# Kernel optimization log

Hardware: AMD Instinct MI355X
Metric: run time of the kernel (lower is better)

The kernel has to match this reference:

```python
import jax, jax.numpy as jnp
import numpy as np

BATCH, SEQ = 256, 100
DM = 256           # d_m
DI = 512           # Mamba d_inner = 2*d_m
DID = 512          # decoder d_inner = 2*d_d
N = 16             # d_state
DTR = 16           # dt_rank = ceil(d_m/16)
DCONV = 4
NLAYERS = 3


def silu(v):
    return v * jax.nn.sigmoid(v)


def setup_inputs() -> dict:
    key = jax.random.key(0)
    ks = jax.random.split(key, 20)
    rn = lambda k, s, sc=0.02: jax.random.normal(k, s, jnp.float32) * sc
    A_log = jnp.log(jnp.arange(1, N + 1, dtype=jnp.float32))  # (N,)
    return {
        'x': jax.random.normal(ks[0], (BATCH, SEQ, 8), jnp.float32),
        'W_embed': rn(ks[1], (8, DM)), 'b_embed': jnp.zeros((DM,), jnp.float32),
        'm_in_w': rn(ks[2], (DM, 2 * DI)),
        'm_conv_w': rn(ks[3], (DI, DCONV), 0.1), 'm_conv_b': jnp.zeros((DI,), jnp.float32),
        'm_xproj_w': rn(ks[4], (DI, DTR + 2 * N)),
        'm_dtproj_w': rn(ks[5], (DTR, DI), DTR ** -0.5),
        'm_dtproj_b': rn(ks[6], (DI,), 0.5) - 4.0,
        'm_A_log': jnp.broadcast_to(A_log, (DI, N)).copy(),
        'm_D': jnp.ones((DI,), jnp.float32),
        'm_out_w': rn(ks[7], (DI, DM)),
        'dec_in_w': rn(ks[8], (NLAYERS, 4, 2 * DID)), 'dec_in_b': jnp.zeros((NLAYERS, 2 * DID), jnp.float32),
        'dec_flow_w': rn(ks[9], (NLAYERS, DM, DTR + 2 * N)),
        'dec_dt_w': rn(ks[10], (NLAYERS, DTR, DID), DTR ** -0.5),
        'dec_dt_b': rn(ks[11], (NLAYERS, DID), 0.5) - 4.0,
        'dec_A_log': jnp.broadcast_to(A_log, (NLAYERS, DID, N)).copy(),
        'dec_D': jnp.ones((NLAYERS, DID), jnp.float32),
        'dec_out_w': rn(ks[12], (NLAYERS, DID, 4)), 'dec_out_b': jnp.zeros((NLAYERS, 4), jnp.float32),
    }


def _forward(x, W_embed, b_embed, m_in_w, m_conv_w, m_conv_b, m_xproj_w,
             m_dtproj_w, m_dtproj_b, m_A_log, m_D, m_out_w,
             dec_in_w, dec_in_b, dec_flow_w, dec_dt_w, dec_dt_b,
             dec_A_log, dec_D, dec_out_w, dec_out_b):
    b, l, _ = x.shape
    # ---- MambaEncoder ----
    emb = x @ W_embed + b_embed                       # (b, l, dm)
    xz = emb @ m_in_w                                 # (b, l, 2*di)
    xs, z = jnp.split(xz, 2, axis=-1)
    # causal depthwise conv1d, kernel=DCONV
    xp = jnp.pad(xs, ((0, 0), (DCONV - 1, 0), (0, 0)))
    xc = sum(xp[:, k:k + l, :] * m_conv_w[:, k] for k in range(DCONV)) + m_conv_b
    xc = silu(xc)
    proj = xc @ m_xproj_w                             # (b, l, dtr+2n)
    dt = jax.nn.softplus(proj[..., :DTR] @ m_dtproj_w + m_dtproj_b)  # (b, l, di)
    Bm = proj[..., DTR:DTR + N]                       # (b, l, n)
    Cm = proj[..., DTR + N:]
    A = -jnp.exp(m_A_log)                             # (di, n)

    def enc_step(h, inp):
        dt_t, B_t, C_t, x_t = inp                     # (b,di),(b,n),(b,n),(b,di)
        h = h * jnp.exp(dt_t[:, :, None] * A) + (dt_t * x_t)[:, :, None] * B_t[:, None, :]
        y = jnp.einsum('bdn,bn->bd', h, C_t) + m_D * x_t
        return h, y

    h0 = jnp.zeros((b, DI, N), xc.dtype)
    _, ys = jax.lax.scan(enc_step, h0,
                         (dt.transpose(1, 0, 2), Bm.transpose(1, 0, 2),
                          Cm.transpose(1, 0, 2), xc.transpose(1, 0, 2)))
    y = ys.transpose(1, 0, 2) * silu(z)               # (b, l, di)
    enc = y @ m_out_w                                 # (b, l, dm)
    flow = enc[:, -1]                                 # (b, dm) -- last token (no cls_token)

    # ---- FlowDecoder stack ----
    cur_bbox = x[:, -1, :4]
    hidden = jnp.zeros((b, DID, N), x.dtype)

    def dec_step(carry, p):
        bbox, h = carry
        in_w, in_b, flow_w, dt_w, dt_b, A_log, Dp, out_w, out_b = p
        bh = bbox @ in_w + in_b                       # (b, 2*did)
        e, r = jnp.split(bh, 2, axis=-1)
        e = silu(e)
        pf = flow @ flow_w                            # (b, dtr+2n)
        dtd = jax.nn.softplus(pf[:, :DTR] @ dt_w + dt_b)  # (b, did)
        Bp, Cp = pf[:, DTR:DTR + N], pf[:, DTR + N:]
        Ad = -jnp.exp(A_log)                          # (did, n)
        h = h * jnp.exp(dtd[:, :, None] * Ad) + e[:, :, None] * (dtd[:, :, None] * Bp[:, None, :])
        yd = jnp.einsum('bdn,bn->bd', h, Cp) + Dp * e
        yd = yd * silu(r)
        out = yd @ out_w + out_b                      # (b, 4)
        # torch code detaches cur_bbox and hidden_state between layers
        return (jax.lax.stop_gradient(out), jax.lax.stop_gradient(h)), out

    _, outs = jax.lax.scan(dec_step, (cur_bbox, hidden),
                           (dec_in_w, dec_in_b, dec_flow_w, dec_dt_w, dec_dt_b,
                            dec_A_log, dec_D, dec_out_w, dec_out_b))
    return outs[-1]                                   # final predicted bbox (b, 4)


def reference(x, W_embed, b_embed, m_in_w, m_conv_w, m_conv_b, m_xproj_w,
              m_dtproj_w, m_dtproj_b, m_A_log, m_D, m_out_w,
              dec_in_w, dec_in_b, dec_flow_w, dec_dt_w, dec_dt_b,
              dec_A_log, dec_D, dec_out_w, dec_out_b):
    return _forward(x, W_embed, b_embed, m_in_w, m_conv_w, m_conv_b, m_xproj_w,
                    m_dtproj_w, m_dtproj_b, m_A_log, m_D, m_out_w,
                    dec_in_w, dec_in_b, dec_flow_w, dec_dt_w, dec_dt_b,
                    dec_A_log, dec_D, dec_out_w, dec_out_b)
```

## Files before the change

kernel.cpp:

```cpp
#include <hip/hip_runtime.h>
#include <math.h>

#define BATCH 256
#define SEQ 100
#define DMODEL 256
#define DI 512
#define DID 512
#define NST 16
#define DTRANK 16
#define DCONV 4
#define NLAYERS 3

#define W2_OFF 0
#define B2_OFF 8192
#define WT_OFF 9216
#define CWT_OFF 33792
#define FLAG_OFF 35840
#define PROJ_OFF 35848
#define SILUZ_OFF 1264648
#define Y_OFF 1395720

__device__ __forceinline__ float silu_f(float x) { return x / (1.0f + __expf(-x)); }
__device__ __forceinline__ float softplus_f(float x) {
    return fmaxf(x, 0.0f) + __logf(1.0f + __expf(-fabsf(x)));
}

#define DPP_ADD(v, ctrl, rmask) \
    v += __int_as_float(__builtin_amdgcn_update_dpp(0, __float_as_int(v), ctrl, rmask, 0xF, false))

__device__ __forceinline__ float wave64_sum(float v) {
    DPP_ADD(v, 0xB1, 0xF);
    DPP_ADD(v, 0x4E, 0xF);
    DPP_ADD(v, 0x141, 0xF);
    DPP_ADD(v, 0x140, 0xF);
    DPP_ADD(v, 0x142, 0xA);
    DPP_ADD(v, 0x143, 0xC);
    return v;
}

__global__ void k_prep(const float* __restrict__ W_embed, const float* __restrict__ b_embed,
                       const float* __restrict__ m_in_w, const float* __restrict__ xproj_w,
                       const float* __restrict__ conv_w, const float* __restrict__ A_log,
                       const float* __restrict__ dec_A_log, float* __restrict__ ws,
                       int* __restrict__ flags) {
    int bid = blockIdx.x, tid = threadIdx.x;
    if (bid < 4) {
        int j = bid * 256 + tid;
        float acc[8] = {0, 0, 0, 0, 0, 0, 0, 0};
        float accb = 0.f;
        for (int c = 0; c < DMODEL; ++c) {
            float w = m_in_w[c * 1024 + j];
            accb += b_embed[c] * w;
#pragma unroll
            for (int i = 0; i < 8; ++i) acc[i] += W_embed[i * DMODEL + c] * w;
        }
#pragma unroll
        for (int i = 0; i < 8; ++i) ws[W2_OFF + i * 1024 + j] = acc[i];
        ws[B2_OFF + j] = accb;
    } else if (bid < 100) {
        int idx = (bid - 4) * 256 + tid;
        int j = idx / 512, c = idx % 512;
        ws[WT_OFF + j * 512 + c] = xproj_w[c * 48 + j];
    } else if (bid < 108) {
        int idx = (bid - 100) * 256 + tid;
        int tap = idx / 512, c = idx % 512;
        ws[CWT_OFF + tap * 512 + c] = conv_w[c * 4 + tap];
    } else {
        __shared__ int oks[2];
        if (tid == 0) { oks[0] = 1; oks[1] = 1; }
        __syncthreads();
        int bad_e = 0, bad_d = 0;
        for (int i = tid; i < DI * NST; i += 256) {
            int dd = i / NST, n = i % NST;
            float a0 = __expf(A_log[dd * NST]);
            float an = __expf(A_log[dd * NST + n]);
            if (fabsf(an - (n + 1) * a0) > 1e-4f * (n + 1)) bad_e = 1;
        }
        for (int i = tid; i < NLAYERS * DID * NST; i += 256) {
            int dd = i / NST, n = i % NST;
            float a0 = __expf(dec_A_log[dd * NST]);
            float an = __expf(dec_A_log[dd * NST + n]);
            if (fabsf(an - (n + 1) * a0) > 1e-4f * (n + 1)) bad_d = 1;
        }
        if (bad_e) atomicAnd(&oks[0], 0);
        if (bad_d) atomicAnd(&oks[1], 0);
        __syncthreads();
        if (tid == 0) { flags[0] = oks[0]; flags[1] = oks[1]; }
    }
}

__global__ void __launch_bounds__(256, 3) k_convproj(
    const float* __restrict__ x, const float* __restrict__ ws, const float* __restrict__ conv_b,
    float* __restrict__ proj_g, float* __restrict__ silu_z) {
    __shared__ __align__(16) float xs_s[23 * 512];
    __shared__ __align__(16) float proj_s[20 * 48];
    const float* W2 = ws + W2_OFF;
    const float* b2 = ws + B2_OFF;
    const float* wT = ws + WT_OFF;
    const float* cwT = ws + CWT_OFF;
    const int b = blockIdx.x / 5, tb = blockIdx.x % 5, t0 = tb * 20;
    const int tid = threadIdx.x, lane = tid & 63, wv = tid >> 6;

    {
        int c0 = tid, c1 = tid + 256;
        float wa[8], wb[8];
#pragma unroll
        for (int i = 0; i < 8; ++i) {
            wa[i] = W2[i * 1024 + c0];
            wb[i] = W2[i * 1024 + c1];
        }
        float ba = b2[c0], bbv = b2[c1];
        for (int r = 0; r < 23; ++r) {
            int t = t0 - 3 + r;
            float va = 0.f, vb = 0.f;
            if (t >= 0) {
                const float4* xr = (const float4*)(x + (size_t)(b * SEQ + t) * 8);
                float4 xlo = xr[0], xhi = xr[1];
                va = ba + xlo.x * wa[0] + xlo.y * wa[1] + xlo.z * wa[2] + xlo.w * wa[3] +
                     xhi.x * wa[4] + xhi.y * wa[5] + xhi.z * wa[6] + xhi.w * wa[7];
                vb = bbv + xlo.x * wb[0] + xlo.y * wb[1] + xlo.z * wb[2] + xlo.w * wb[3] +
                     xhi.x * wb[4] + xhi.y * wb[5] + xhi.z * wb[6] + xhi.w * wb[7];
            }
            xs_s[r * 512 + c0] = va;
            xs_s[r * 512 + c1] = vb;
        }
        if (tb == 4) {
            const float4* xr = (const float4*)(x + (size_t)(b * SEQ + SEQ - 1) * 8);
            float4 xlo = xr[0], xhi = xr[1];
            float za = b2[512 + c0], zb = b2[512 + c1];
#pragma unroll
            for (int i = 0; i < 8; ++i) {
                float xi = (i < 4) ? ((const float*)&xlo)[i] : ((const float*)&xhi)[i - 4];
                za += xi * W2[i * 1024 + 512 + c0];
                zb += xi * W2[i * 1024 + 512 + c1];
            }
            silu_z[b * DI + c0] = silu_f(za);
            silu_z[b * DI + c1] = silu_f(zb);
        }
    }
    __syncthreads();
    {
        float cwr[8][4], cbr[8];
#pragma unroll
        for (int k = 0; k < 8; ++k) {
            int c = lane + 64 * k;
#pragma unroll
            for (int tap = 0; tap < 4; ++tap) cwr[k][tap] = cwT[tap * 512 + c];
            cbr[k] = conv_b[c];
        }
        float xcv[5][8];
#pragma unroll
        for (int q = 0; q < 5; ++q) {
            int rb = wv * 5 + q;
#pragma unroll
            for (int k = 0; k < 8; ++k) {
                int c = lane + 64 * k;
                float a = cbr[k];
#pragma unroll
                for (int tap = 0; tap < 4; ++tap) a += cwr[k][tap] * xs_s[(rb + tap) * 512 + c];
                xcv[q][k] = silu_f(a);
            }
        }
        for (int j = 0; j < 48; ++j) {
            float wj[8];
#pragma unroll
            for (int k = 0; k < 8; ++k) wj[k] = wT[j * 512 + lane + 64 * k];
            float a0 = 0, a1 = 0, a2 = 0, a3 = 0, a4 = 0;
#pragma unroll
            for (int k = 0; k < 8; ++k) {
                float w = wj[k];
                a0 += xcv[0][k] * w;
                a1 += xcv[1][k] * w;
                a2 += xcv[2][k] * w;
                a3 += xcv[3][k] * w;
                a4 += xcv[4][k] * w;
            }
            a0 = wave64_sum(a0); a1 = wave64_sum(a1); a2 = wave64_sum(a2);
            a3 = wave64_sum(a3); a4 = wave64_sum(a4);
            if (lane == 63) {
                proj_s[(wv * 5 + 0) * 48 + j] = a0;
                proj_s[(wv * 5 + 1) * 48 + j] = a1;
                proj_s[(wv * 5 + 2) * 48 + j] = a2;
                proj_s[(wv * 5 + 3) * 48 + j] = a3;
                proj_s[(wv * 5 + 4) * 48 + j] = a4;
            }
        }
    }
    __syncthreads();
    if (tid < 240) {
        float4* dst = (float4*)(proj_g + (size_t)(b * SEQ + t0) * 48);
        dst[tid] = ((const float4*)proj_s)[tid];
    }
}

__global__ void __launch_bounds__(512, 4) k_scan(
    const float* __restrict__ x, const float* __restrict__ ws, const float* __restrict__ conv_b,
    const float* __restrict__ proj_g, const float* __restrict__ A_log,
    const float* __restrict__ dtw, const float* __restrict__ dtb,
    const float* __restrict__ Dvec, const float* __restrict__ silu_z,
    const int* __restrict__ flags, float* __restrict__ y_g) {
    __shared__ __align__(16) float proj_l[SEQ * 48];
    __shared__ __align__(16) float x_l[SEQ * 8];
    __shared__ __align__(16) float h1_s[256 * 16];
    const int b = blockIdx.x >> 1, dgrp = blockIdx.x & 1;
    const int tid = threadIdx.x, half = tid >> 8, dl = tid & 255;
    const int d = dgrp * 256 + dl;
    const float* W2 = ws + W2_OFF;
    const float* b2 = ws + B2_OFF;
    const float* cwT = ws + CWT_OFF;

    for (int i = tid; i < SEQ * 48; i += 512) proj_l[i] = proj_g[(size_t)b * SEQ * 48 + i];
    for (int i = tid; i < SEQ * 8; i += 512) x_l[i] = x[(size_t)b * SEQ * 8 + i];

    float w2c[8];
#pragma unroll
    for (int i = 0; i < 8; ++i) w2c[i] = W2[i * 1024 + d];
    float biasc = b2[d];
    float cw0 = cwT[d], cw1 = cwT[512 + d], cw2 = cwT[1024 + d], cw3 = cwT[1536 + d];
    float cb = conv_b[d];
    float wr[DTRANK];
#pragma unroll
    for (int r = 0; r < DTRANK; ++r) wr[r] = dtw[r * DI + d];
    float bdt = dtb[d];
    float An0 = -__expf(A_log[d * NST]);
    const bool fast = flags[0] != 0;
    float h[NST];
#pragma unroll
    for (int n = 0; n < NST; ++n) h[n] = 0.f;
    float S = 0.f, xcv = 0.f;
    const int tstart = half * 50, tend = tstart + 50;
    __syncthreads();

    float win0 = 0.f, win1 = 0.f, win2 = 0.f;
    for (int tt = tstart - 3; tt < tstart; ++tt) {
        float v = 0.f;
        if (tt >= 0) {
            const float4* xr = (const float4*)&x_l[tt * 8];
            float4 xa = xr[0], xb4 = xr[1];
            v = biasc + xa.x * w2c[0] + xa.y * w2c[1] + xa.z * w2c[2] + xa.w * w2c[3] +
                xb4.x * w2c[4] + xb4.y * w2c[5] + xb4.z * w2c[6] + xb4.w * w2c[7];
        }
        win0 = win1; win1 = win2; win2 = v;
    }

    for (int t = tstart; t < tend; ++t) {
        const float4* xr = (const float4*)&x_l[t * 8];
        float4 xa = xr[0], xb4 = xr[1];
        float xsv = biasc + xa.x * w2c[0] + xa.y * w2c[1] + xa.z * w2c[2] + xa.w * w2c[3] +
                    xb4.x * w2c[4] + xb4.y * w2c[5] + xb4.z * w2c[6] + xb4.w * w2c[7];
        float cv = cb + win0 * cw0 + win1 * cw1 + win2 * cw2 + xsv * cw3;
        win0 = win1; win1 = win2; win2 = xsv;
        xcv = silu_f(cv);
        const float* pr = &proj_l[t * 48];
        float4 p0 = *(const float4*)&pr[0];
        float4 p1 = *(const float4*)&pr[4];
        float4 p2 = *(const float4*)&pr[8];
        float4 p3 = *(const float4*)&pr[12];
        float acc = bdt;
        acc += p0.x * wr[0] + p0.y * wr[1] + p0.z * wr[2] + p0.w * wr[3];
        acc += p1.x * wr[4] + p1.y * wr[5] + p1.z * wr[6] + p1.w * wr[7];
        acc += p2.x * wr[8] + p2.y * wr[9] + p2.z * wr[10] + p2.w * wr[11];
        acc += p3.x * wr[12] + p3.y * wr[13] + p3.z * wr[14] + p3.w * wr[15];
        float dtv = softplus_f(acc);
        S += dtv;
        float s = dtv * xcv;
        float4 B0 = *(const float4*)&pr[16];
        float4 B1 = *(const float4*)&pr[20];
        float4 B2 = *(const float4*)&pr[24];
        float4 B3 = *(const float4*)&pr[28];
        float Bv[NST] = {B0.x, B0.y, B0.z, B0.w, B1.x, B1.y, B1.z, B1.w,
                         B2.x, B2.y, B2.z, B2.w, B3.x, B3.y, B3.z, B3.w};
        if (fast) {
            float E = __expf(dtv * An0);
            float Ek = 1.f;
#pragma unroll
            for (int n = 0; n < NST; ++n) {
                Ek *= E;
                h[n] = h[n] * Ek + s * Bv[n];
            }
        } else {
#pragma unroll
            for (int n = 0; n < NST; ++n) {
                float Ann = -__expf(A_log[d * NST + n]);
                h[n] = h[n] * __expf(dtv * Ann) + s * Bv[n];
            }
        }
    }
    if (half == 0) {
#pragma unroll
        for (int n = 0; n < NST; n += 4)
            *(float4*)&h1_s[dl * 16 + n] = make_float4(h[n], h[n + 1], h[n + 2], h[n + 3]);
    }
    __syncthreads();
    if (half == 1) {
        const float* pr = &proj_l[(SEQ - 1) * 48];
        float yv = Dvec[d] * xcv;
        if (fast) {
            float Gb = __expf(S * An0), Gk = 1.f;
#pragma unroll
            for (int n = 0; n < NST; ++n) {
                Gk *= Gb;
                float hf = h[n] + Gk * h1_s[dl * 16 + n];
                yv += hf * pr[32 + n];
            }
        } else {
#pragma unroll
            for (int n = 0; n < NST; ++n) {
                float Ann = -__expf(A_log[d * NST + n]);
                float hf = h[n] + __expf(S * Ann) * h1_s[dl * 16 + n];
                yv += hf * pr[32 + n];
            }
        }
        y_g[(size_t)b * DI + d] = yv * silu_z[(size_t)b * DI + d];
    }
}

__global__ void __launch_bounds__(512, 2) k_flowdec(
    const float* __restrict__ x, const float* __restrict__ y_g,
    const float* __restrict__ m_out_w, const float* __restrict__ dec_in_w,
    const float* __restrict__ dec_in_b, const float* __restrict__ dec_flow_w,
    const float* __restrict__ dec_dt_w, const float* __restrict__ dec_dt_b,
    const float* __restrict__ dec_A_log, const float* __restrict__ dec_D,
    const float* __restrict__ dec_out_w, const float* __restrict__ dec_out_b,
    const int* __restrict__ flags, float* __restrict__ out) {
    __shared__ __align__(16) float y_s[DI];
    __shared__ __align__(16) float pf_s[48];
    __shared__ float red_s[DMODEL];
    __shared__ float flow_s[DMODEL];
    __shared__ float bbox_s[4];
    __shared__ float dred_s[8][4];
    const int b = blockIdx.x, tid = threadIdx.x, d = tid;
    const int lane = tid & 63, wv = tid >> 6;
    const bool dfast = flags[1] != 0;
    y_s[d] = y_g[(size_t)b * DI + d];
    if (tid < 4) bbox_s[tid] = x[(size_t)(b * SEQ + SEQ - 1) * 8 + tid];
    __syncthreads();
    {
        int j = tid >> 1, p = tid & 1;
        float fa = 0.f;
#pragma unroll 4
        for (int i = 0; i < 64; ++i) {
            int c = p * 256 + 4 * i;
            float4 yq = *(const float4*)&y_s[c];
            fa += yq.x * m_out_w[(c + 0) * DMODEL + j];
            fa += yq.y * m_out_w[(c + 1) * DMODEL + j];
            fa += yq.z * m_out_w[(c + 2) * DMODEL + j];
            fa += yq.w * m_out_w[(c + 3) * DMODEL + j];
        }
        if (p == 1) red_s[j] = fa;
        __syncthreads();
        if (p == 0) flow_s[j] = fa + red_s[j];
    }
    float h[NST];
#pragma unroll
    for (int n = 0; n < NST; ++n) h[n] = 0.f;
    __syncthreads();
    for (int L = 0; L < NLAYERS; ++L) {
        float epre = dec_in_b[L * 1024 + d];
        float rpre = dec_in_b[L * 1024 + 512 + d];
#pragma unroll
        for (int i = 0; i < 4; ++i) {
            float bx = bbox_s[i];
            epre += bx * dec_in_w[(L * 4 + i) * 1024 + d];
            rpre += bx * dec_in_w[(L * 4 + i) * 1024 + 512 + d];
        }
        float e = silu_f(epre);
        float fl4[4];
#pragma unroll
        for (int k = 0; k < 4; ++k) fl4[k] = flow_s[lane + 64 * k];
        float pj[6];
#pragma unroll
        for (int jj = 0; jj < 6; ++jj) {
            float a = 0.f;
#pragma unroll
            for (int k = 0; k < 4; ++k)
                a += fl4[k] * dec_flow_w[L * DMODEL * 48 + (lane + 64 * k) * 48 + wv * 6 + jj];
            pj[jj] = wave64_sum(a);
        }
        if (lane == 63) {
#pragma unroll
            for (int jj = 0; jj < 6; ++jj) pf_s[wv * 6 + jj] = pj[jj];
        }
        __syncthreads();
        float4 p0 = *(const float4*)&pf_s[0];
        float4 p1 = *(const float4*)&pf_s[4];
        float4 p2 = *(const float4*)&pf_s[8];
        float4 p3 = *(const float4*)&pf_s[12];
        float dtd = dec_dt_b[L * DID + d];
        dtd += p0.x * dec_dt_w[(L * 16 + 0) * DID + d] + p0.y * dec_dt_w[(L * 16 + 1) * DID + d] +
               p0.z * dec_dt_w[(L * 16 + 2) * DID + d] + p0.w * dec_dt_w[(L * 16 + 3) * DID + d];
        dtd += p1.x * dec_dt_w[(L * 16 + 4) * DID + d] + p1.y * dec_dt_w[(L * 16 + 5) * DID + d] +
               p1.z * dec_dt_w[(L * 16 + 6) * DID + d] + p1.w * dec_dt_w[(L * 16 + 7) * DID + d];
        dtd += p2.x * dec_dt_w[(L * 16 + 8) * DID + d] + p2.y * dec_dt_w[(L * 16 + 9) * DID + d] +
               p2.z * dec_dt_w[(L * 16 + 10) * DID + d] + p2.w * dec_dt_w[(L * 16 + 11) * DID + d];
        dtd += p3.x * dec_dt_w[(L * 16 + 12) * DID + d] + p3.y * dec_dt_w[(L * 16 + 13) * DID + d] +
               p3.z * dec_dt_w[(L * 16 + 14) * DID + d] + p3.w * dec_dt_w[(L * 16 + 15) * DID + d];
        dtd = softplus_f(dtd);
        float4 B0 = *(const float4*)&pf_s[16];
        float4 B1 = *(const float4*)&pf_s[20];
        float4 B2 = *(const float4*)&pf_s[24];
        float4 B3 = *(const float4*)&pf_s[28];
        float4 C0 = *(const float4*)&pf_s[32];
        float4 C1 = *(const float4*)&pf_s[36];
        float4 C2 = *(const float4*)&pf_s[40];
        float4 C3 = *(const float4*)&pf_s[44];
        float Bv[NST] = {B0.x, B0.y, B0.z, B0.w, B1.x, B1.y, B1.z, B1.w,
                         B2.x, B2.y, B2.z, B2.w, B3.x, B3.y, B3.z, B3.w};
        float Cv[NST] = {C0.x, C0.y, C0.z, C0.w, C1.x, C1.y, C1.z, C1.w,
                         C2.x, C2.y, C2.z, C2.w, C3.x, C3.y, C3.z, C3.w};
        float yd = 0.f;
        if (dfast) {
            float Ad0 = -__expf(dec_A_log[(L * DID + d) * NST]);
            float E = __expf(dtd * Ad0), Ek = 1.f;
#pragma unroll
            for (int n = 0; n < NST; ++n) {
                Ek *= E;
                h[n] = h[n] * Ek + e * (dtd * Bv[n]);
                yd += h[n] * Cv[n];
            }
        } else {
#pragma unroll
            for (int n = 0; n < NST; ++n) {
                float Adn = -__expf(dec_A_log[(L * DID + d) * NST + n]);
                h[n] = h[n] * __expf(dtd * Adn) + e * (dtd * Bv[n]);
                yd += h[n] * Cv[n];
            }
        }
        yd += dec_D[L * DID + d] * e;
        yd *= silu_f(rpre);
#pragma unroll
        for (int jo = 0; jo < 4; ++jo) {
            float v = wave64_sum(yd * dec_out_w[(L * DID + d) * 4 + jo]);
            if (lane == 63) dred_s[wv][jo] = v;
        }
        __syncthreads();
        if (tid < 4) {
            float a2 = dec_out_b[L * 4 + tid];
#pragma unroll
            for (int w = 0; w < 8; ++w) a2 += dred_s[w][tid];
            bbox_s[tid] = a2;
            if (L == NLAYERS - 1) out[b * 4 + tid] = a2;
        }
        __syncthreads();
    }
}

extern "C" void kernel_launch(void* const* d_in, const int* in_sizes, int n_in,
                              void* d_out, int out_size, void* d_ws, size_t ws_size,
                              hipStream_t stream) {
    const float* x          = (const float*)d_in[0];
    const float* W_embed    = (const float*)d_in[1];
    const float* b_embed    = (const float*)d_in[2];
    const float* m_in_w     = (const float*)d_in[3];
    const float* m_conv_w   = (const float*)d_in[4];
    const float* m_conv_b   = (const float*)d_in[5];
    const float* m_xproj_w  = (const float*)d_in[6];
    const float* m_dtproj_w = (const float*)d_in[7];
    const float* m_dtproj_b = (const float*)d_in[8];
    const float* m_A_log    = (const float*)d_in[9];
    const float* m_D        = (const float*)d_in[10];
    const float* m_out_w    = (const float*)d_in[11];
    const float* dec_in_w   = (const float*)d_in[12];
    const float* dec_in_b   = (const float*)d_in[13];
    const float* dec_flow_w = (const float*)d_in[14];
    const float* dec_dt_w   = (const float*)d_in[15];
    const float* dec_dt_b   = (const float*)d_in[16];
    const float* dec_A_log  = (const float*)d_in[17];
    const float* dec_D      = (const float*)d_in[18];
    const float* dec_out_w  = (const float*)d_in[19];
    const float* dec_out_b  = (const float*)d_in[20];

    float* ws = (float*)d_ws;
    int* flags = (int*)(ws + FLAG_OFF);
    float* proj_g = ws + PROJ_OFF;
    float* siluz = ws + SILUZ_OFF;
    float* y_g = ws + Y_OFF;

    k_prep<<<109, 256, 0, stream>>>(W_embed, b_embed, m_in_w, m_xproj_w, m_conv_w,
                                    m_A_log, dec_A_log, ws, flags);
    k_convproj<<<BATCH * 5, 256, 0, stream>>>(x, ws, m_conv_b, proj_g, siluz);
    k_scan<<<BATCH * 2, 512, 0, stream>>>(x, ws, m_conv_b, proj_g, m_A_log, m_dtproj_w,
                                          m_dtproj_b, m_D, siluz, flags, y_g);
    k_flowdec<<<BATCH, 512, 0, stream>>>(x, y_g, m_out_w, dec_in_w, dec_in_b, dec_flow_w,
                                         dec_dt_w, dec_dt_b, dec_A_log, dec_D, dec_out_w,
                                         dec_out_b, flags, (float*)d_out);
}
```

Baseline: 155.0 us.

## Stream scan operands via scalar loads, vectorize convproj, tree power chains

The scan kernel no longer stages proj and x in shared memory. It streams each timestep's projection row and input row into SGPRs with double-buffered inline-asm s_load instructions, removing the block-wide staging and the barrier before the scan. The conv/projection kernel switches to float2/float4 vectorized loads and LDS accesses with a new channel-to-lane mapping. The serial Ek*=E power chains are replaced by a tree of products to shorten dependency chains, softplus is simplified to a thresholded form, and the h1_s buffer is padded to 17 floats per row to avoid bank conflicts. Hand-written asm with manual lgkmcnt waits adds fragility and SGPR pressure, and the softplus threshold slightly changes numerics.

```diff
diff --git a/kernel.cpp b/kernel.cpp
--- a/kernel.cpp
+++ b/kernel.cpp
@@ -21,9 +21,6 @@
 #define Y_OFF 1395720
 
 __device__ __forceinline__ float silu_f(float x) { return x / (1.0f + __expf(-x)); }
-__device__ __forceinline__ float softplus_f(float x) {
-    return fmaxf(x, 0.0f) + __logf(1.0f + __expf(-fabsf(x)));
-}
 
 #define DPP_ADD(v, ctrl, rmask) \
     v += __int_as_float(__builtin_amdgcn_update_dpp(0, __float_as_int(v), ctrl, rmask, 0xF, false))
@@ -37,6 +34,26 @@
     DPP_ADD(v, 0x143, 0xC);
     return v;
 }
+
+typedef float sf16 __attribute__((ext_vector_type(16)));
+typedef float sf8 __attribute__((ext_vector_type(8)));
+
+__device__ __forceinline__ int rfl(int v) { return __builtin_amdgcn_readfirstlane(v); }
+
+#define SL2(dA, dB, base, offA, offB)                    \
+    asm volatile("s_load_dwordx16 %0, %2, %3\n\t"        \
+                 "s_load_dwordx16 %1, %2, %4"            \
+                 : "=&s"(dA), "=&s"(dB)                  \
+                 : "s"(base), "s"(offA), "s"(offB))
+#define SLX(dX, base, off) \
+    asm volatile("s_load_dwordx8 %0, %1, %2" : "=&s"(dX) : "s"(base), "s"(off))
+#define SLC(dC, base, off) \
+    asm volatile("s_load_dwordx16 %0, %1, %2" : "=&s"(dC) : "s"(base), "s"(off))
+#define SL_WAIT()                                          \
+    do {                                                   \
+        asm volatile("s_waitcnt lgkmcnt(0)" ::: "memory"); \
+        __builtin_amdgcn_sched_barrier(0);                 \
+    } while (0)
 
 __global__ void k_prep(const float* __restrict__ W_embed, const float* __restrict__ b_embed,
                        const float* __restrict__ m_in_w, const float* __restrict__ xproj_w,
@@ -102,78 +119,89 @@
     const int tid = threadIdx.x, lane = tid & 63, wv = tid >> 6;
 
     {
-        int c0 = tid, c1 = tid + 256;
+        int c0 = tid * 2;
         float wa[8], wb[8];
 #pragma unroll
         for (int i = 0; i < 8; ++i) {
-            wa[i] = W2[i * 1024 + c0];
-            wb[i] = W2[i * 1024 + c1];
-        }
-        float ba = b2[c0], bbv = b2[c1];
+            float2 wp = *(const float2*)&W2[i * 1024 + c0];
+            wa[i] = wp.x;
+            wb[i] = wp.y;
+        }
+        float2 bp = *(const float2*)&b2[c0];
         for (int r = 0; r < 23; ++r) {
             int t = t0 - 3 + r;
             float va = 0.f, vb = 0.f;
             if (t >= 0) {
                 const float4* xr = (const float4*)(x + (size_t)(b * SEQ + t) * 8);
                 float4 xlo = xr[0], xhi = xr[1];
-                va = ba + xlo.x * wa[0] + xlo.y * wa[1] + xlo.z * wa[2] + xlo.w * wa[3] +
+                va = bp.x + xlo.x * wa[0] + xlo.y * wa[1] + xlo.z * wa[2] + xlo.w * wa[3] +
                      xhi.x * wa[4] + xhi.y * wa[5] + xhi.z * wa[6] + xhi.w * wa[7];
-                vb = bbv + xlo.x * wb[0] + xlo.y * wb[1] + xlo.z * wb[2] + xlo.w * wb[3] +
+                vb = bp.y + xlo.x * wb[0] + xlo.y * wb[1] + xlo.z * wb[2] + xlo.w * wb[3] +
                      xhi.x * wb[4] + xhi.y * wb[5] + xhi.z * wb[6] + xhi.w * wb[7];
             }
-            xs_s[r * 512 + c0] = va;
-            xs_s[r * 512 + c1] = vb;
+            *(float2*)&xs_s[r * 512 + c0] = make_float2(va, vb);
         }
         if (tb == 4) {
             const float4* xr = (const float4*)(x + (size_t)(b * SEQ + SEQ - 1) * 8);
             float4 xlo = xr[0], xhi = xr[1];
-            float za = b2[512 + c0], zb = b2[512 + c1];
+            float za = b2[512 + c0], zb = b2[512 + c0 + 1];
 #pragma unroll
             for (int i = 0; i < 8; ++i) {
                 float xi = (i < 4) ? ((const float*)&xlo)[i] : ((const float*)&xhi)[i - 4];
-                za += xi * W2[i * 1024 + 512 + c0];
-                zb += xi * W2[i * 1024 + 512 + c1];
+                float2 wp = *(const float2*)&W2[i * 1024 + 512 + c0];
+                za += xi * wp.x;
+                zb += xi * wp.y;
             }
             silu_z[b * DI + c0] = silu_f(za);
-            silu_z[b * DI + c1] = silu_f(zb);
+            silu_z[b * DI + c0 + 1] = silu_f(zb);
         }
     }
     __syncthreads();
+    const int cA = lane * 4, cB = 256 + lane * 4;
+    float xcv[5][8];
     {
-        float cwr[8][4], cbr[8];
-#pragma unroll
-        for (int k = 0; k < 8; ++k) {
-            int c = lane + 64 * k;
-#pragma unroll
-            for (int tap = 0; tap < 4; ++tap) cwr[k][tap] = cwT[tap * 512 + c];
-            cbr[k] = conv_b[c];
-        }
-        float xcv[5][8];
+        float4 cwA[4], cwB[4];
+#pragma unroll
+        for (int tap = 0; tap < 4; ++tap) {
+            cwA[tap] = *(const float4*)&cwT[tap * 512 + cA];
+            cwB[tap] = *(const float4*)&cwT[tap * 512 + cB];
+        }
+        float4 cbA = *(const float4*)&conv_b[cA];
+        float4 cbB = *(const float4*)&conv_b[cB];
 #pragma unroll
         for (int q = 0; q < 5; ++q) {
             int rb = wv * 5 + q;
-#pragma unroll
-            for (int k = 0; k < 8; ++k) {
-                int c = lane + 64 * k;
-                float a = cbr[k];
-#pragma unroll
-                for (int tap = 0; tap < 4; ++tap) a += cwr[k][tap] * xs_s[(rb + tap) * 512 + c];
-                xcv[q][k] = silu_f(a);
-            }
-        }
+            float4 aA = cbA, aB = cbB;
+#pragma unroll
+            for (int tap = 0; tap < 4; ++tap) {
+                float4 xA = *(const float4*)&xs_s[(rb + tap) * 512 + cA];
+                float4 xB = *(const float4*)&xs_s[(rb + tap) * 512 + cB];
+                aA.x += cwA[tap].x * xA.x; aA.y += cwA[tap].y * xA.y;
+                aA.z += cwA[tap].z * xA.z; aA.w += cwA[tap].w * xA.w;
+                aB.x += cwB[tap].x * xB.x; aB.y += cwB[tap].y * xB.y;
+                aB.z += cwB[tap].z * xB.z; aB.w += cwB[tap].w * xB.w;
+            }
+            xcv[q][0] = silu_f(aA.x); xcv[q][1] = silu_f(aA.y);
+            xcv[q][2] = silu_f(aA.z); xcv[q][3] = silu_f(aA.w);
+            xcv[q][4] = silu_f(aB.x); xcv[q][5] = silu_f(aB.y);
+            xcv[q][6] = silu_f(aB.z); xcv[q][7] = silu_f(aB.w);
+        }
+    }
+    {
+#pragma unroll 2
         for (int j = 0; j < 48; ++j) {
-            float wj[8];
-#pragma unroll
-            for (int k = 0; k < 8; ++k) wj[k] = wT[j * 512 + lane + 64 * k];
-            float a0 = 0, a1 = 0, a2 = 0, a3 = 0, a4 = 0;
-#pragma unroll
-            for (int k = 0; k < 8; ++k) {
-                float w = wj[k];
-                a0 += xcv[0][k] * w;
-                a1 += xcv[1][k] * w;
-                a2 += xcv[2][k] * w;
-                a3 += xcv[3][k] * w;
-                a4 += xcv[4][k] * w;
+            float4 wA = *(const float4*)&wT[j * 512 + cA];
+            float4 wB = *(const float4*)&wT[j * 512 + cB];
+            float a0 = 0.f, a1 = 0.f, a2 = 0.f, a3 = 0.f, a4 = 0.f;
+#pragma unroll
+            for (int k = 0; k < 4; ++k) {
+                float wk = ((const float*)&wA)[k];
+                float wk2 = ((const float*)&wB)[k];
+                a0 += xcv[0][k] * wk + xcv[0][4 + k] * wk2;
+                a1 += xcv[1][k] * wk + xcv[1][4 + k] * wk2;
+                a2 += xcv[2][k] * wk + xcv[2][4 + k] * wk2;
+                a3 += xcv[3][k] * wk + xcv[3][4 + k] * wk2;
+                a4 += xcv[4][k] * wk + xcv[4][4 + k] * wk2;
             }
             a0 = wave64_sum(a0); a1 = wave64_sum(a1); a2 = wave64_sum(a2);
             a3 = wave64_sum(a3); a4 = wave64_sum(a4);
@@ -193,24 +221,66 @@
     }
 }
 
+#define SCAN_STEP(SA, SB, SX)                                                        \
+    do {                                                                             \
+        float xsv = biasc;                                                           \
+        xsv = fmaf((SX)[0], w2c[0], xsv); xsv = fmaf((SX)[1], w2c[1], xsv);          \
+        xsv = fmaf((SX)[2], w2c[2], xsv); xsv = fmaf((SX)[3], w2c[3], xsv);          \
+        xsv = fmaf((SX)[4], w2c[4], xsv); xsv = fmaf((SX)[5], w2c[5], xsv);          \
+        xsv = fmaf((SX)[6], w2c[6], xsv); xsv = fmaf((SX)[7], w2c[7], xsv);          \
+        float cv = cb + win0 * cw0 + win1 * cw1 + win2 * cw2 + xsv * cw3;            \
+        win0 = win1; win1 = win2; win2 = xsv;                                        \
+        xcv = silu_f(cv);                                                            \
+        float acc = bdt;                                                             \
+        acc = fmaf((SA)[0], wr[0], acc);  acc = fmaf((SA)[1], wr[1], acc);           \
+        acc = fmaf((SA)[2], wr[2], acc);  acc = fmaf((SA)[3], wr[3], acc);           \
+        acc = fmaf((SA)[4], wr[4], acc);  acc = fmaf((SA)[5], wr[5], acc);           \
+        acc = fmaf((SA)[6], wr[6], acc);  acc = fmaf((SA)[7], wr[7], acc);           \
+        acc = fmaf((SA)[8], wr[8], acc);  acc = fmaf((SA)[9], wr[9], acc);           \
+        acc = fmaf((SA)[10], wr[10], acc); acc = fmaf((SA)[11], wr[11], acc);        \
+        acc = fmaf((SA)[12], wr[12], acc); acc = fmaf((SA)[13], wr[13], acc);        \
+        acc = fmaf((SA)[14], wr[14], acc); acc = fmaf((SA)[15], wr[15], acc);        \
+        float dtv = (acc > 20.f) ? acc : __logf(1.f + __expf(acc));                  \
+        S += dtv;                                                                    \
+        float sv = dtv * xcv;                                                        \
+        if (fast) {                                                                  \
+            float E1 = __expf(dtv * An0);                                            \
+            float E2 = E1 * E1, E3 = E2 * E1, E4 = E2 * E2;                          \
+            float E5 = E4 * E1, E6 = E4 * E2, E7 = E4 * E3, E8 = E4 * E4;            \
+            float E9 = E8 * E1, E10 = E8 * E2, E11 = E8 * E3, E12 = E8 * E4;         \
+            float E13 = E8 * E5, E14 = E8 * E6, E15 = E8 * E7, E16 = E8 * E8;        \
+            h[0] = fmaf(h[0], E1, sv * (SB)[0]);   h[1] = fmaf(h[1], E2, sv * (SB)[1]); \
+            h[2] = fmaf(h[2], E3, sv * (SB)[2]);   h[3] = fmaf(h[3], E4, sv * (SB)[3]); \
+            h[4] = fmaf(h[4], E5, sv * (SB)[4]);   h[5] = fmaf(h[5], E6, sv * (SB)[5]); \
+            h[6] = fmaf(h[6], E7, sv * (SB)[6]);   h[7] = fmaf(h[7], E8, sv * (SB)[7]); \
+            h[8] = fmaf(h[8], E9, sv * (SB)[8]);   h[9] = fmaf(h[9], E10, sv * (SB)[9]); \
+            h[10] = fmaf(h[10], E11, sv * (SB)[10]); h[11] = fmaf(h[11], E12, sv * (SB)[11]); \
+            h[12] = fmaf(h[12], E13, sv * (SB)[12]); h[13] = fmaf(h[13], E14, sv * (SB)[13]); \
+            h[14] = fmaf(h[14], E15, sv * (SB)[14]); h[15] = fmaf(h[15], E16, sv * (SB)[15]); \
+        } else {                                                                     \
+            _Pragma("unroll")                                                        \
+            for (int n = 0; n < NST; ++n) {                                          \
+                float Ann = -__expf(A_log[d * NST + n]);                             \
+                h[n] = fmaf(h[n], __expf(dtv * Ann), sv * (SB)[n]);                  \
+            }                                                                        \
+        }                                                                            \
+    } while (0)
+
 __global__ void __launch_bounds__(512, 4) k_scan(
     const float* __restrict__ x, const float* __restrict__ ws, const float* __restrict__ conv_b,
     const float* __restrict__ proj_g, const float* __restrict__ A_log,
     const float* __restrict__ dtw, const float* __restrict__ dtb,
     const float* __restrict__ Dvec, const float* __restrict__ silu_z,
     const int* __restrict__ flags, float* __restrict__ y_g) {
-    __shared__ __align__(16) float proj_l[SEQ * 48];
-    __shared__ __align__(16) float x_l[SEQ * 8];
-    __shared__ __align__(16) float h1_s[256 * 16];
+    __shared__ float h1_s[256 * 17];
     const int b = blockIdx.x >> 1, dgrp = blockIdx.x & 1;
     const int tid = threadIdx.x, half = tid >> 8, dl = tid & 255;
     const int d = dgrp * 256 + dl;
     const float* W2 = ws + W2_OFF;
     const float* b2 = ws + B2_OFF;
     const float* cwT = ws + CWT_OFF;
-
-    for (int i = tid; i < SEQ * 48; i += 512) proj_l[i] = proj_g[(size_t)b * SEQ * 48 + i];
-    for (int i = tid; i < SEQ * 8; i += 512) x_l[i] = x[(size_t)b * SEQ * 8 + i];
+    const float* proj_b = proj_g + (size_t)b * SEQ * 48;
+    const float* x_b = x + (size_t)b * SEQ * 8;
 
     float w2c[8];
 #pragma unroll
@@ -228,14 +298,13 @@
 #pragma unroll
     for (int n = 0; n < NST; ++n) h[n] = 0.f;
     float S = 0.f, xcv = 0.f;
-    const int tstart = half * 50, tend = tstart + 50;
-    __syncthreads();
+    const int tstart = half * 50;
 
     float win0 = 0.f, win1 = 0.f, win2 = 0.f;
     for (int tt = tstart - 3; tt < tstart; ++tt) {
         float v = 0.f;
         if (tt >= 0) {
-            const float4* xr = (const float4*)&x_l[tt * 8];
+            const float4* xr = (const float4*)(x_b + tt * 8);
             float4 xa = xr[0], xb4 = xr[1];
             v = biasc + xa.x * w2c[0] + xa.y * w2c[1] + xa.z * w2c[2] + xa.w * w2c[3] +
                 xb4.x * w2c[4] + xb4.y * w2c[5] + xb4.z * w2c[6] + xb4.w * w2c[7];
@@ -243,72 +312,58 @@
         win0 = win1; win1 = win2; win2 = v;
     }
 
-    for (int t = tstart; t < tend; ++t) {
-        const float4* xr = (const float4*)&x_l[t * 8];
-        float4 xa = xr[0], xb4 = xr[1];
-        float xsv = biasc + xa.x * w2c[0] + xa.y * w2c[1] + xa.z * w2c[2] + xa.w * w2c[3] +
-                    xb4.x * w2c[4] + xb4.y * w2c[5] + xb4.z * w2c[6] + xb4.w * w2c[7];
-        float cv = cb + win0 * cw0 + win1 * cw1 + win2 * cw2 + xsv * cw3;
-        win0 = win1; win1 = win2; win2 = xsv;
-        xcv = silu_f(cv);
-        const float* pr = &proj_l[t * 48];
-        float4 p0 = *(const float4*)&pr[0];
-        float4 p1 = *(const float4*)&pr[4];
-        float4 p2 = *(const float4*)&pr[8];
-        float4 p3 = *(const float4*)&pr[12];
-        float acc = bdt;
-        acc += p0.x * wr[0] + p0.y * wr[1] + p0.z * wr[2] + p0.w * wr[3];
-        acc += p1.x * wr[4] + p1.y * wr[5] + p1.z * wr[6] + p1.w * wr[7];
-        acc += p2.x * wr[8] + p2.y * wr[9] + p2.z * wr[10] + p2.w * wr[11];
-        acc += p3.x * wr[12] + p3.y * wr[13] + p3.z * wr[14] + p3.w * wr[15];
-        float dtv = softplus_f(acc);
-        S += dtv;
-        float s = dtv * xcv;
-        float4 B0 = *(const float4*)&pr[16];
-        float4 B1 = *(const float4*)&pr[20];
-        float4 B2 = *(const float4*)&pr[24];
-        float4 B3 = *(const float4*)&pr[28];
-        float Bv[NST] = {B0.x, B0.y, B0.z, B0.w, B1.x, B1.y, B1.z, B1.w,
-                         B2.x, B2.y, B2.z, B2.w, B3.x, B3.y, B3.z, B3.w};
+    int poff = rfl(tstart * 192);
+    int xoff = rfl(tstart * 32);
+    sf16 a0, a1, b0, b1;
+    sf8 ax, bx;
+    SL2(a0, a1, proj_b, poff, poff + 64);
+    SLX(ax, x_b, xoff);
+    SL_WAIT();
+    for (int it = 0; it < 25; ++it) {
+        int p1 = poff + 192, x1 = xoff + 32;
+        SL2(b0, b1, proj_b, p1, p1 + 64);
+        SLX(bx, x_b, x1);
+        SCAN_STEP(a0, a1, ax);
+        SL_WAIT();
+        int p2 = (it < 24) ? poff + 384 : p1;
+        int x2 = (it < 24) ? xoff + 64 : x1;
+        SL2(a0, a1, proj_b, p2, p2 + 64);
+        SLX(ax, x_b, x2);
+        SCAN_STEP(b0, b1, bx);
+        SL_WAIT();
+        poff += 384;
+        xoff += 64;
+    }
+
+    if (half == 0) {
+#pragma unroll
+        for (int n = 0; n < NST; ++n) h1_s[dl * 17 + n] = h[n];
+    }
+    __syncthreads();
+    if (half == 1) {
+        sf16 cC;
+        SLC(cC, proj_b, (SEQ - 1) * 192 + 128);
+        SL_WAIT();
+        float yv = Dvec[d] * xcv;
         if (fast) {
-            float E = __expf(dtv * An0);
-            float Ek = 1.f;
+            float G1 = __expf(S * An0);
+            float G2 = G1 * G1, G3 = G2 * G1, G4 = G2 * G2;
+            float G5 = G4 * G1, G6 = G4 * G2, G7 = G4 * G3, G8 = G4 * G4;
+            float G9 = G8 * G1, G10 = G8 * G2, G11 = G8 * G3, G12 = G8 * G4;
+            float G13 = G8 * G5, G14 = G8 * G6, G15 = G8 * G7, G16 = G8 * G8;
+            float Gs[NST] = {G1, G2, G3, G4, G5, G6, G7, G8,
+                             G9, G10, G11, G12, G13, G14, G15, G16};
 #pragma unroll
             for (int n = 0; n < NST; ++n) {
-                Ek *= E;
-                h[n] = h[n] * Ek + s * Bv[n];
+                float hf = fmaf(h1_s[dl * 17 + n], Gs[n], h[n]);
+                yv = fmaf(hf, cC[n], yv);
             }
         } else {
 #pragma unroll
             for (int n = 0; n < NST; ++n) {
                 float Ann = -__expf(A_log[d * NST + n]);
-                h[n] = h[n] * __expf(dtv * Ann) + s * Bv[n];
-            }
-        }
-    }
-    if (half == 0) {
-#pragma unroll
-        for (int n = 0; n < NST; n += 4)
-            *(float4*)&h1_s[dl * 16 + n] = make_float4(h[n], h[n + 1], h[n + 2], h[n + 3]);
-    }
-    __syncthreads();
-    if (half == 1) {
-        const float* pr = &proj_l[(SEQ - 1) * 48];
-        float yv = Dvec[d] * xcv;
-        if (fast) {
-            float Gb = __expf(S * An0), Gk = 1.f;
-#pragma unroll
-            for (int n = 0; n < NST; ++n) {
-                Gk *= Gb;
-                float hf = h[n] + Gk * h1_s[dl * 16 + n];
-                yv += hf * pr[32 + n];
-            }
-        } else {
-#pragma unroll
-            for (int n = 0; n < NST; ++n) {
-                float Ann = -__expf(A_log[d * NST + n]);
-                float hf = h[n] + __expf(S * Ann) * h1_s[dl * 16 + n];
-                yv += hf * pr[32 + n];
+                float hf = fmaf(h1_s[dl * 17 + n], __expf(S * Ann), h[n]);
+                yv = fmaf(hf, cC[n], yv);
             }
         }
         y_g[(size_t)b * DI + d] = yv * silu_z[(size_t)b * DI + d];
@@ -395,7 +450,7 @@
                p2.z * dec_dt_w[(L * 16 + 10) * DID + d] + p2.w * dec_dt_w[(L * 16 + 11) * DID + d];
         dtd += p3.x * dec_dt_w[(L * 16 + 12) * DID + d] + p3.y * dec_dt_w[(L * 16 + 13) * DID + d] +
                p3.z * dec_dt_w[(L * 16 + 14) * DID + d] + p3.w * dec_dt_w[(L * 16 + 15) * DID + d];
-        dtd = softplus_f(dtd);
+        dtd = (dtd > 20.f) ? dtd : __logf(1.f + __expf(dtd));
         float4 B0 = *(const float4*)&pf_s[16];
         float4 B1 = *(const float4*)&pf_s[20];
         float4 B2 = *(const float4*)&pf_s[24];
@@ -411,18 +466,23 @@
         float yd = 0.f;
         if (dfast) {
             float Ad0 = -__expf(dec_A_log[(L * DID + d) * NST]);
-            float E = __expf(dtd * Ad0), Ek = 1.f;
+            float E1 = __expf(dtd * Ad0);
+            float E2 = E1 * E1, E3 = E2 * E1, E4 = E2 * E2;
+            float E5 = E4 * E1, E6 = E4 * E2, E7 = E4 * E3, E8 = E4 * E4;
+            float E9 = E8 * E1, E10 = E8 * E2, E11 = E8 * E3, E12 = E8 * E4;
+            float E13 = E8 * E5, E14 = E8 * E6, E15 = E8 * E7, E16 = E8 * E8;
+            float Es[NST] = {E1, E2, E3, E4, E5, E6, E7, E8,
+                             E9, E10, E11, E12, E13, E14, E15, E16};
 #pragma unroll
             for (int n = 0; n < NST; ++n) {
-                Ek *= E;
-                h[n] = h[n] * Ek + e * (dtd * Bv[n]);
+                h[n] = fmaf(h[n], Es[n], e * (dtd * Bv[n]));
                 yd += h[n] * Cv[n];
             }
         } else {
 #pragma unroll
             for (int n = 0; n < NST; ++n) {
                 float Adn = -__expf(dec_A_log[(L * DID + d) * NST + n]);
-                h[n] = h[n] * __expf(dtd * Adn) + e * (dtd * Bv[n]);
+                h[n] = fmaf(h[n], __expf(dtd * Adn), e * (dtd * Bv[n]));
                 yd += h[n] * Cv[n];
             }
         }
```

New measurement: 148.5 us. 1.04x faster.
